# Optimization experiments

Measured on AMD Instinct MI355X. Metric: run time of the kernel, lower is better.

Reference implementation:

```python
import jax, jax.numpy as jnp
import numpy as np

N, E, EP, DIN, H = 100000, 600000, 100000, 128, 128


def _lin_params(key, din, dout):
    k1, k2 = jax.random.split(key)
    bound = 1.0 / np.sqrt(din)
    W = jax.random.uniform(k1, (din, dout), minval=-bound, maxval=bound, dtype=jnp.float32)
    b = jax.random.uniform(k2, (dout,), minval=-bound, maxval=bound, dtype=jnp.float32)
    return W, b


def setup_inputs() -> dict:
    key = jax.random.key(0)
    ks = jax.random.split(key, 12)
    x = jax.random.normal(ks[0], (N, DIN), dtype=jnp.float32)
    edge_attr = jax.random.normal(ks[1], (E, 1), dtype=jnp.float32)
    edge_index = jax.random.randint(ks[2], (2, E), 0, N, dtype=jnp.int64)
    predict_edge_index = jax.random.randint(ks[3], (2, EP), 0, N, dtype=jnp.int64)
    W1, b1 = _lin_params(ks[4], DIN, H)          # GCNConv layer 0
    W2, b2 = _lin_params(ks[5], H, H)            # GCNConv layer 1
    eW1, eb1 = _lin_params(ks[6], H + H + 1, H)  # edge_mlp layer 0
    eW2, eb2 = _lin_params(ks[7], H + H + H, H)  # edge_mlp layer 1
    pW1, pb1 = _lin_params(ks[8], 2 * H, H)      # edge_mlps2
    pW2, pb2 = _lin_params(ks[9], H, H)
    pW3, pb3 = _lin_params(ks[10], H, H)
    pW4, pb4 = _lin_params(ks[11], H, 1)
    return dict(x=x, edge_attr=edge_attr, edge_index=edge_index,
                predict_edge_index=predict_edge_index,
                W1=W1, b1=b1, W2=W2, b2=b2, eW1=eW1, eb1=eb1, eW2=eW2, eb2=eb2,
                pW1=pW1, pb1=pb1, pW2=pW2, pb2=pb2, pW3=pW3, pb3=pb3, pW4=pW4, pb4=pb4)


def _gcn_conv(x, edge_index, W, b):
    # PyG GCNConv: add self-loops, symmetric normalization, aggregate at target.
    src, dst = edge_index[0], edge_index[1]
    loop = jnp.arange(N)
    src2 = jnp.concatenate([src, loop])
    dst2 = jnp.concatenate([dst, loop])
    deg = jax.ops.segment_sum(jnp.ones_like(dst2, dtype=x.dtype), dst2, num_segments=N)
    dinv = jnp.where(deg > 0, jax.lax.rsqrt(deg), 0.0)
    norm = dinv[src2] * dinv[dst2]                 # [E+N]
    h = x @ W                                      # [N, H]
    msg = norm[:, None] * h[src2]                  # gather + scale
    return jax.ops.segment_sum(msg, dst2, num_segments=N) + b


def reference(x, edge_attr, edge_index, predict_edge_index,
              W1, b1, W2, b2, eW1, eb1, eW2, eb2,
              pW1, pb1, pW2, pb2, pW3, pb3, pW4, pb4):
    # layer 0
    x = jax.nn.relu(_gcn_conv(x, edge_index, W1, b1))
    xi, xj = x[edge_index[0]], x[edge_index[1]]
    edge_attr = jax.nn.relu(jnp.concatenate([xi, xj, edge_attr], axis=-1) @ eW1 + eb1)
    # (Sequential already has ReLU; forward applies relu again -- idempotent)
    # layer 1
    x = jax.nn.relu(_gcn_conv(x, edge_index, W2, b2))
    xi, xj = x[edge_index[0]], x[edge_index[1]]
    edge_attr = jax.nn.relu(jnp.concatenate([xi, xj, edge_attr], axis=-1) @ eW2 + eb2)
    # predict_edge
    xi, xj = x[predict_edge_index[0]], x[predict_edge_index[1]]
    y = jnp.concatenate([xi, xj], axis=-1)
    y = jax.nn.relu(y @ pW1 + pb1)
    y = jax.nn.relu(y @ pW2 + pb2)
    y = jax.nn.relu(y @ pW3 + pb3)
    y = jax.nn.relu(y @ pW4 + pb4)
    return y
```

## Files before the change

### kernel.cpp

```cpp
#include <hip/hip_runtime.h>

typedef __attribute__((ext_vector_type(8))) short bf16x8;
typedef __attribute__((ext_vector_type(4))) float f32x4;
typedef __attribute__((ext_vector_type(16))) float f32x16;
typedef __attribute__((ext_vector_type(2))) float f32x2;

__device__ __forceinline__ unsigned bfr16(float x) {
    unsigned u = __float_as_uint(x);
    return (u + 0x7fffu + ((u >> 16) & 1u)) >> 16;
}

union U8 { bf16x8 v; unsigned u[4]; };

__device__ __forceinline__ void frag_from_f32(const float* fp, bf16x8& hi) {
    float4 f0 = *(const float4*)fp;
    float4 f1 = *(const float4*)(fp + 4);
    float fv[8] = {f0.x, f0.y, f0.z, f0.w, f1.x, f1.y, f1.z, f1.w};
    U8 H;
    #pragma unroll
    for (int p = 0; p < 4; p++)
        H.u[p] = bfr16(fv[2 * p]) | (bfr16(fv[2 * p + 1]) << 16);
    hi = H.v;
}

__device__ __forceinline__ bf16x8 frag_from_f8(const unsigned char* p) {
    uint2 q = *(const uint2*)p;
    f32x2 e0 = __builtin_amdgcn_cvt_pk_f32_fp8(q.x, false);
    f32x2 e1 = __builtin_amdgcn_cvt_pk_f32_fp8(q.x, true);
    f32x2 e2 = __builtin_amdgcn_cvt_pk_f32_fp8(q.y, false);
    f32x2 e3 = __builtin_amdgcn_cvt_pk_f32_fp8(q.y, true);
    U8 H;
    H.u[0] = bfr16(e0.x) | (bfr16(e0.y) << 16);
    H.u[1] = bfr16(e1.x) | (bfr16(e1.y) << 16);
    H.u[2] = bfr16(e2.x) | (bfr16(e2.y) << 16);
    H.u[3] = bfr16(e3.x) | (bfr16(e3.y) << 16);
    return H.v;
}

__device__ __forceinline__ void stage_w512(unsigned short* sm, const unsigned short* Wp, int t) {
    const uint4* src = (const uint4*)Wp;
    uint4* dst = (uint4*)sm;
    #pragma unroll
    for (int p = 0; p < 4; p++) dst[t + p * 512] = src[t + p * 512];
}

__device__ __forceinline__ bf16x8 wfrag_lds(const unsigned short* sm, int f, int lane) {
    return *(const bf16x8*)(sm + f * 512 + lane * 8);
}


__device__ __forceinline__ bf16x8 trans32(const f32x16& A, int sb, float4 bva, float4 bvb) {
    float v0 = fmaxf(A[sb + 0] + bva.x, 0.f);
    float v1 = fmaxf(A[sb + 1] + bva.y, 0.f);
    float v2 = fmaxf(A[sb + 2] + bva.z, 0.f);
    float v3 = fmaxf(A[sb + 3] + bva.w, 0.f);
    float v4 = fmaxf(A[sb + 4] + bvb.x, 0.f);
    float v5 = fmaxf(A[sb + 5] + bvb.y, 0.f);
    float v6 = fmaxf(A[sb + 6] + bvb.z, 0.f);
    float v7 = fmaxf(A[sb + 7] + bvb.w, 0.f);
    U8 H;
    H.u[0] = bfr16(v0) | (bfr16(v1) << 16);
    H.u[1] = bfr16(v2) | (bfr16(v3) << 16);
    H.u[2] = bfr16(v4) | (bfr16(v5) << 16);
    H.u[3] = bfr16(v6) | (bfr16(v7) << 16);
    return H.v;
}


__global__ void zero1_k(int* __restrict__ a, int n) {
    int i = blockIdx.x * blockDim.x + threadIdx.x;
    if (i < n) a[i] = 0;
}

__global__ void hist_k(const int* __restrict__ dst, int* __restrict__ deg,
                       int* __restrict__ rank, int E) {
    int e = blockIdx.x * blockDim.x + threadIdx.x;
    if (e < E) rank[e] = atomicAdd(&deg[dst[e]], 1);
}

__global__ void scan1_k(const int* __restrict__ deg, int* __restrict__ rowptr,
                        int* __restrict__ bsum, float* __restrict__ dinv, int n) {
    __shared__ int s[256];
    int tid = threadIdx.x;
    int i = blockIdx.x * 256 + tid;
    int v = (i < n) ? deg[i] : 0;
    s[tid] = v;
    __syncthreads();
    #pragma unroll
    for (int off = 1; off < 256; off <<= 1) {
        int t = (tid >= off) ? s[tid - off] : 0;
        __syncthreads();
        s[tid] += t;
        __syncthreads();
    }
    if (i < n) {
        rowptr[i] = s[tid] - v;
        dinv[i] = rsqrtf((float)(v + 1));
    }
    if (tid == 255) bsum[blockIdx.x] = s[255];
}

__global__ void scan2_k(int* __restrict__ bsum, int nb) {
    __shared__ int s[512];
    int tid = threadIdx.x;
    int v = (tid < nb) ? bsum[tid] : 0;
    s[tid] = v;
    __syncthreads();
    #pragma unroll
    for (int off = 1; off < 512; off <<= 1) {
        int t = (tid >= off) ? s[tid - off] : 0;
        __syncthreads();
        s[tid] += t;
        __syncthreads();
    }
    if (tid < nb) bsum[tid] = s[tid] - v;
}

__global__ void place_k(const int* __restrict__ src, const int* __restrict__ dst,
                        const int* __restrict__ rowptr, const int* __restrict__ bsum,
                        const int* __restrict__ rank, int* __restrict__ csr, int E) {
    int e = blockIdx.x * blockDim.x + threadIdx.x;
    if (e < E) {
        int d = dst[e];
        int pos = rowptr[d] + bsum[d >> 8] + rank[e];
        csr[pos] = src[e];
    }
}

__global__ void wprep6_k(const float* __restrict__ s0, const float* __restrict__ s1,
                         const float* __restrict__ s2, const float* __restrict__ s3,
                         const float* __restrict__ s4, const float* __restrict__ s5,
                         unsigned short* __restrict__ dstBase) {
    const float* W;
    switch (blockIdx.y) {
        case 0: W = s0; break; case 1: W = s1; break; case 2: W = s2; break;
        case 3: W = s3; break; case 4: W = s4; break; default: W = s5; break;
    }
    unsigned short* out = dstBase + (size_t)blockIdx.y * 16384;
    int idx = blockIdx.x * 256 + threadIdx.x;
    if (idx >= 16384) return;
    int k = idx >> 7, c = idx & 127;
    unsigned hr = bfr16(W[k * 128 + c]);
    int pos;
    if (blockIdx.y < 2) {
        int kt = k >> 5, gk = (k >> 3) & 3, j = k & 7;
        int nt = ((c >> 5) << 1) | ((c >> 2) & 1);
        int rho = (((c >> 3) & 3) << 2) | (c & 3);
        int lane = (gk << 4) | rho;
        pos = (kt * 8 + nt) * 512 + lane * 8 + j;
    } else {
        int kk = k >> 4, gk = (k >> 3) & 1, jj = k & 7;
        int ktc = c >> 4, hc = (c >> 3) & 1, jc = c & 7;
        int n = ktc >> 1;
        int reg = ((ktc & 1) << 3) | jc;
        int m = (reg & 3) + 8 * (reg >> 2) + 4 * hc;
        int lane = (gk << 5) | m;
        pos = (kk * 4 + n) * 512 + lane * 8 + jj;
    }
    out[pos] = (unsigned short)hr;
}

#define ACC16(Q)                                                              \
    {                                                                         \
        f32x2 e;                                                              \
        e = __builtin_amdgcn_cvt_pk_f32_fp8((Q).x, false); a0 += e.x; a1 += e.y; \
        e = __builtin_amdgcn_cvt_pk_f32_fp8((Q).x, true);  a2 += e.x; a3 += e.y; \
        e = __builtin_amdgcn_cvt_pk_f32_fp8((Q).y, false); a4 += e.x; a5 += e.y; \
        e = __builtin_amdgcn_cvt_pk_f32_fp8((Q).y, true);  a6 += e.x; a7 += e.y; \
        e = __builtin_amdgcn_cvt_pk_f32_fp8((Q).z, false); a8 += e.x; a9 += e.y; \
        e = __builtin_amdgcn_cvt_pk_f32_fp8((Q).z, true);  a10 += e.x; a11 += e.y; \
        e = __builtin_amdgcn_cvt_pk_f32_fp8((Q).w, false); a12 += e.x; a13 += e.y; \
        e = __builtin_amdgcn_cvt_pk_f32_fp8((Q).w, true);  a14 += e.x; a15 += e.y; \
    }

template<int OUTFMT>
__global__ __launch_bounds__(256)
void gather8_k(const unsigned char* __restrict__ hp, const float* __restrict__ dinv,
               const int* __restrict__ rowptr, const int* __restrict__ bsum,
               const int* __restrict__ deg, const int* __restrict__ csr,
               const float* __restrict__ bias, void* __restrict__ outPtr, int N)
{
    int tid = threadIdx.x;
    int lane = tid & 63;
    int grp = lane >> 3, cl = lane & 7;
    int i = blockIdx.x * 32 + (tid >> 6) * 8 + grp;
    if (i >= N) return;
    int c16 = cl * 16;
    uint4 p = *(const uint4*)(hp + (size_t)i * 128 + c16);
    float a0 = 0.f, a1 = 0.f, a2 = 0.f, a3 = 0.f, a4 = 0.f, a5 = 0.f, a6 = 0.f, a7 = 0.f;
    float a8 = 0.f, a9 = 0.f, a10 = 0.f, a11 = 0.f, a12 = 0.f, a13 = 0.f, a14 = 0.f, a15 = 0.f;
    ACC16(p);
    int beg = rowptr[i] + bsum[i >> 8];
    int dg = deg[i];
    int j = 0;
    for (; j + 7 < dg; j += 8) {
        uint4 q[8];
        #pragma unroll
        for (int u = 0; u < 8; u++) {
            int su = csr[beg + j + u];
            q[u] = *(const uint4*)(hp + (size_t)su * 128 + c16);
        }
        #pragma unroll
        for (int u = 0; u < 8; u++) ACC16(q[u]);
    }
    for (; j + 3 < dg; j += 4) {
        uint4 q[4];
        #pragma unroll
        for (int u = 0; u < 4; u++) {
            int su = csr[beg + j + u];
            q[u] = *(const uint4*)(hp + (size_t)su * 128 + c16);
        }
        #pragma unroll
        for (int u = 0; u < 4; u++) ACC16(q[u]);
    }
    for (; j < dg; j++) {
        int su = csr[beg + j];
        uint4 q0 = *(const uint4*)(hp + (size_t)su * 128 + c16);
        ACC16(q0);
    }
    float di = dinv[i];
    float4 b0 = *(const float4*)(bias + c16);
    float4 b1 = *(const float4*)(bias + c16 + 4);
    float4 b2 = *(const float4*)(bias + c16 + 8);
    float4 b3 = *(const float4*)(bias + c16 + 12);
    float v0  = fmaxf(b0.x + di * a0,  0.f), v1  = fmaxf(b0.y + di * a1,  0.f);
    float v2  = fmaxf(b0.z + di * a2,  0.f), v3  = fmaxf(b0.w + di * a3,  0.f);
    float v4  = fmaxf(b1.x + di * a4,  0.f), v5  = fmaxf(b1.y + di * a5,  0.f);
    float v6  = fmaxf(b1.z + di * a6,  0.f), v7  = fmaxf(b1.w + di * a7,  0.f);
    float v8  = fmaxf(b2.x + di * a8,  0.f), v9  = fmaxf(b2.y + di * a9,  0.f);
    float v10 = fmaxf(b2.z + di * a10, 0.f), v11 = fmaxf(b2.w + di * a11, 0.f);
    float v12 = fmaxf(b3.x + di * a12, 0.f), v13 = fmaxf(b3.y + di * a13, 0.f);
    float v14 = fmaxf(b3.z + di * a14, 0.f), v15 = fmaxf(b3.w + di * a15, 0.f);
    if (OUTFMT == 0) {
        unsigned short* outp = (unsigned short*)outPtr + (size_t)i * 128 + c16;
        uint4 o0, o1;
        o0.x = bfr16(v0)  | (bfr16(v1)  << 16);
        o0.y = bfr16(v2)  | (bfr16(v3)  << 16);
        o0.z = bfr16(v4)  | (bfr16(v5)  << 16);
        o0.w = bfr16(v6)  | (bfr16(v7)  << 16);
        o1.x = bfr16(v8)  | (bfr16(v9)  << 16);
        o1.y = bfr16(v10) | (bfr16(v11) << 16);
        o1.z = bfr16(v12) | (bfr16(v13) << 16);
        o1.w = bfr16(v14) | (bfr16(v15) << 16);
        *(uint4*)outp = o0;
        *(uint4*)(outp + 8) = o1;
    } else {
        int r0 = 0, r1 = 0, r2 = 0, r3 = 0;
        r0 = __builtin_amdgcn_cvt_pk_fp8_f32(v0,  v1,  r0, false);
        r0 = __builtin_amdgcn_cvt_pk_fp8_f32(v2,  v3,  r0, true);
        r1 = __builtin_amdgcn_cvt_pk_fp8_f32(v4,  v5,  r1, false);
        r1 = __builtin_amdgcn_cvt_pk_fp8_f32(v6,  v7,  r1, true);
        r2 = __builtin_amdgcn_cvt_pk_fp8_f32(v8,  v9,  r2, false);
        r2 = __builtin_amdgcn_cvt_pk_fp8_f32(v10, v11, r2, true);
        r3 = __builtin_amdgcn_cvt_pk_fp8_f32(v12, v13, r3, false);
        r3 = __builtin_amdgcn_cvt_pk_fp8_f32(v14, v15, r3, true);
        uint4 o = make_uint4((unsigned)r0, (unsigned)r1, (unsigned)r2, (unsigned)r3);
        *(uint4*)((unsigned char*)outPtr + (size_t)i * 128 + c16) = o;
    }
}

template<int AMODE>
__global__ __launch_bounds__(512)
void rowgemm_k(const void* __restrict__ Asrc, const unsigned short* __restrict__ Wp,
               const float* __restrict__ rowScale, unsigned char* __restrict__ CoutF8, int M)
{
    __shared__ __align__(16) unsigned short smw[16384];
    const int t = threadIdx.x, lane = t & 63, wave = t >> 6;
    const int base = blockIdx.x * 128 + wave * 16;
    const int s = lane & 15, g = lane >> 4, kg = g * 8;
    const int arow = base + s;
    const int rowc = (arow < M) ? arow : (M - 1);

    stage_w512(smw, Wp, t);

    bf16x8 yh[4];
    #pragma unroll
    for (int kt = 0; kt < 4; kt++) {
        if (AMODE == 1)
            yh[kt] = *(const bf16x8*)((const unsigned short*)Asrc + (size_t)rowc * 128 + kt * 32 + kg);
        else
            frag_from_f32((const float*)Asrc + (size_t)rowc * 128 + kt * 32 + kg, yh[kt]);
    }
    __syncthreads();

    f32x4 acc[8];
    #pragma unroll
    for (int nt = 0; nt < 8; nt++) acc[nt] = (f32x4){0.f, 0.f, 0.f, 0.f};

    #pragma unroll
    for (int kt = 0; kt < 4; kt++) {
        #pragma unroll
        for (int nt = 0; nt < 8; nt++) {
            bf16x8 whi = wfrag_lds(smw, kt * 8 + nt, lane);
            acc[nt] = __builtin_amdgcn_mfma_f32_16x16x32_bf16(whi, yh[kt], acc[nt], 0, 0, 0);
        }
    }

    if (arow < M) {
        float sc = rowScale[arow];
        #pragma unroll
        for (int nt = 0; nt < 8; nt++) {
            int cbase = 32 * (nt >> 1) + 8 * g + 4 * (nt & 1);
            int r = 0;
            r = __builtin_amdgcn_cvt_pk_fp8_f32(acc[nt][0] * sc, acc[nt][1] * sc, r, false);
            r = __builtin_amdgcn_cvt_pk_fp8_f32(acc[nt][2] * sc, acc[nt][3] * sc, r, true);
            *(unsigned*)(CoutF8 + (size_t)arow * 128 + cbase) = (unsigned)r;
        }
    }
}

__global__ __launch_bounds__(512)
void mlp_k(const unsigned char* __restrict__ X, const int* __restrict__ psrc, const int* __restrict__ pdst,
           const unsigned short* __restrict__ W1a, const unsigned short* __restrict__ W1b,
           const float* __restrict__ b1, const unsigned short* __restrict__ W2p,
           const float* __restrict__ b2, const unsigned short* __restrict__ W3p,
           const float* __restrict__ b3, const float* __restrict__ w4,
           const float* __restrict__ b4p, float* __restrict__ out, int M)
{
    __shared__ __align__(16) unsigned short smw[2][16384];
    const int t = threadIdx.x, lane = t & 63, wave = t >> 6;
    const int base = blockIdx.x * 256 + wave * 32;
    const int s = lane & 31, h8 = (lane >> 5) * 8;
    const int arow = base + s;
    const int rowc = (arow < M) ? arow : (M - 1);
    const int si = psrc[rowc], sj = pdst[rowc];

    bf16x8 xi[8], xj[8];
    #pragma unroll
    for (int kt = 0; kt < 8; kt++)
        xi[kt] = frag_from_f8(X + (size_t)si * 128 + kt * 16 + h8);
    #pragma unroll
    for (int kt = 0; kt < 8; kt++)
        xj[kt] = frag_from_f8(X + (size_t)sj * 128 + kt * 16 + h8);

    stage_w512(smw[0], W1a, t);
    stage_w512(smw[1], W1b, t);
    __syncthreads();

    f32x16 acc1[4];
    #pragma unroll
    for (int nt = 0; nt < 4; nt++)
        #pragma unroll
        for (int q = 0; q < 16; q++) acc1[nt][q] = 0.f;
    #pragma unroll
    for (int kt = 0; kt < 8; kt++) {
        #pragma unroll
        for (int nt = 0; nt < 4; nt++) {
            bf16x8 wa = wfrag_lds(smw[0], kt * 4 + nt, lane);
            acc1[nt] = __builtin_amdgcn_mfma_f32_32x32x16_bf16(wa, xi[kt], acc1[nt], 0, 0, 0);
            bf16x8 wb = wfrag_lds(smw[1], kt * 4 + nt, lane);
            acc1[nt] = __builtin_amdgcn_mfma_f32_32x32x16_bf16(wb, xj[kt], acc1[nt], 0, 0, 0);
        }
    }
    __syncthreads();

    stage_w512(smw[0], W2p, t);
    stage_w512(smw[1], W3p, t);
    __syncthreads();

    f32x16 acc2[4];
    #pragma unroll
    for (int nt = 0; nt < 4; nt++)
        #pragma unroll
        for (int q = 0; q < 16; q++) acc2[nt][q] = 0.f;
    #pragma unroll
    for (int kt = 0; kt < 8; kt++) {
        float4 bva = *(const float4*)(b1 + kt * 16 + h8);
        float4 bvb = *(const float4*)(b1 + kt * 16 + h8 + 4);
        bf16x8 yh = trans32(acc1[kt >> 1], (kt & 1) * 8, bva, bvb);
        #pragma unroll
        for (int nt = 0; nt < 4; nt++) {
            bf16x8 whi = wfrag_lds(smw[0], kt * 4 + nt, lane);
            acc2[nt] = __builtin_amdgcn_mfma_f32_32x32x16_bf16(whi, yh, acc2[nt], 0, 0, 0);
        }
    }

    f32x16 acc3[4];
    #pragma unroll
    for (int nt = 0; nt < 4; nt++)
        #pragma unroll
        for (int q = 0; q < 16; q++) acc3[nt][q] = 0.f;
    #pragma unroll
    for (int kt = 0; kt < 8; kt++) {
        float4 bva = *(const float4*)(b2 + kt * 16 + h8);
        float4 bvb = *(const float4*)(b2 + kt * 16 + h8 + 4);
        bf16x8 yh = trans32(acc2[kt >> 1], (kt & 1) * 8, bva, bvb);
        #pragma unroll
        for (int nt = 0; nt < 4; nt++) {
            bf16x8 whi = wfrag_lds(smw[1], kt * 4 + nt, lane);
            acc3[nt] = __builtin_amdgcn_mfma_f32_32x32x16_bf16(whi, yh, acc3[nt], 0, 0, 0);
        }
    }

    float p = 0.f;
    #pragma unroll
    for (int nt = 0; nt < 4; nt++) {
        int c1 = 32 * nt + h8;
        int c2 = 32 * nt + 16 + h8;
        float4 b3a = *(const float4*)(b3 + c1);
        float4 b3b = *(const float4*)(b3 + c1 + 4);
        float4 b3c = *(const float4*)(b3 + c2);
        float4 b3d = *(const float4*)(b3 + c2 + 4);
        float4 w4a = *(const float4*)(w4 + c1);
        float4 w4b = *(const float4*)(w4 + c1 + 4);
        float4 w4c = *(const float4*)(w4 + c2);
        float4 w4d = *(const float4*)(w4 + c2 + 4);
        p += fmaxf(acc3[nt][0]  + b3a.x, 0.f) * w4a.x;
        p += fmaxf(acc3[nt][1]  + b3a.y, 0.f) * w4a.y;
        p += fmaxf(acc3[nt][2]  + b3a.z, 0.f) * w4a.z;
        p += fmaxf(acc3[nt][3]  + b3a.w, 0.f) * w4a.w;
        p += fmaxf(acc3[nt][4]  + b3b.x, 0.f) * w4b.x;
        p += fmaxf(acc3[nt][5]  + b3b.y, 0.f) * w4b.y;
        p += fmaxf(acc3[nt][6]  + b3b.z, 0.f) * w4b.z;
        p += fmaxf(acc3[nt][7]  + b3b.w, 0.f) * w4b.w;
        p += fmaxf(acc3[nt][8]  + b3c.x, 0.f) * w4c.x;
        p += fmaxf(acc3[nt][9]  + b3c.y, 0.f) * w4c.y;
        p += fmaxf(acc3[nt][10] + b3c.z, 0.f) * w4c.z;
        p += fmaxf(acc3[nt][11] + b3c.w, 0.f) * w4c.w;
        p += fmaxf(acc3[nt][12] + b3d.x, 0.f) * w4d.x;
        p += fmaxf(acc3[nt][13] + b3d.y, 0.f) * w4d.y;
        p += fmaxf(acc3[nt][14] + b3d.z, 0.f) * w4d.z;
        p += fmaxf(acc3[nt][15] + b3d.w, 0.f) * w4d.w;
    }
    p += __shfl_xor(p, 32, 64);
    if (lane < 32 && arow < M) out[arow] = fmaxf(p + b4p[0], 0.f);
}

extern "C" void kernel_launch(void* const* d_in, const int* in_sizes, int n_in,
                              void* d_out, int out_size, void* d_ws, size_t ws_size,
                              hipStream_t stream)
{
    const float* x   = (const float*)d_in[0];
    const int*   ei  = (const int*)d_in[2];
    const int*   pei = (const int*)d_in[3];
    const float* W1  = (const float*)d_in[4];
    const float* b1  = (const float*)d_in[5];
    const float* W2  = (const float*)d_in[6];
    const float* b2  = (const float*)d_in[7];
    const float* pW1 = (const float*)d_in[12];
    const float* pb1 = (const float*)d_in[13];
    const float* pW2 = (const float*)d_in[14];
    const float* pb2 = (const float*)d_in[15];
    const float* pW3 = (const float*)d_in[16];
    const float* pb3 = (const float*)d_in[17];
    const float* pW4 = (const float*)d_in[18];
    const float* pb4 = (const float*)d_in[19];

    const int N  = in_sizes[0] / 128;
    const int E  = in_sizes[2] / 2;
    const int EP = in_sizes[3] / 2;
    const int Npad = (N + 255) & ~255;

    float*          ws     = (float*)d_ws;
    float*          dinv   = ws;
    unsigned char*  hpF8   = (unsigned char*)(ws + Npad);
    unsigned short* bufB   = (unsigned short*)(hpF8 + (size_t)N * 128);
    unsigned char*  bufC   = (unsigned char*)(bufB + (size_t)N * 128);
    size_t ioff = (((size_t)(bufC + (size_t)N * 128)) + 255) & ~(size_t)255;
    int*   deg    = (int*)ioff;
    int*   rowptr = deg + Npad;
    int*   rank   = rowptr + Npad;
    int*   csr    = rank + E;
    int*   bsum   = csr + E;
    size_t wpOff = ((size_t)(bsum + 512) + 15) & ~(size_t)15;
    unsigned short* wp = (unsigned short*)wpOff;
    unsigned short* W1p  = wp;
    unsigned short* W2p  = wp + 16384;
    unsigned short* P1Ap = wp + 2 * 16384;
    unsigned short* P1Bp = wp + 3 * 16384;
    unsigned short* P2p  = wp + 4 * 16384;
    unsigned short* P3p  = wp + 5 * 16384;
    float* out = (float*)d_out;

    const int* esrc = ei;
    const int* edst = ei + E;
    const int* psrc = pei;
    const int* pdst = pei + EP;

    const int nb = (N + 255) / 256;
    const int gN = (N + 255) / 256;
    const int gE = (E + 255) / 256;
    const int gT = (N + 127) / 128;
    const int gP = (EP + 255) / 256;
    const int gG = (N + 31) / 32;

    zero1_k<<<gN, 256, 0, stream>>>(deg, N);
    hist_k<<<gE, 256, 0, stream>>>(edst, deg, rank, E);
    scan1_k<<<nb, 256, 0, stream>>>(deg, rowptr, bsum, dinv, N);
    scan2_k<<<1, 512, 0, stream>>>(bsum, nb);
    place_k<<<gE, 256, 0, stream>>>(esrc, edst, rowptr, bsum, rank, csr, E);

    wprep6_k<<<dim3(64, 6), 256, 0, stream>>>(W1, W2, pW1, pW1 + 128 * 128, pW2, pW3, wp);

    rowgemm_k<0><<<gT, 512, 0, stream>>>(x, W1p, dinv, hpF8, N);
    gather8_k<0><<<gG, 256, 0, stream>>>(hpF8, dinv, rowptr, bsum, deg, csr, b1, bufB, N);

    rowgemm_k<1><<<gT, 512, 0, stream>>>(bufB, W2p, dinv, hpF8, N);
    gather8_k<1><<<gG, 256, 0, stream>>>(hpF8, dinv, rowptr, bsum, deg, csr, b2, bufC, N);

    mlp_k<<<gP, 512, 0, stream>>>(bufC, psrc, pdst, P1Ap, P1Bp, pb1, P2p, pb2, P3p, pb3,
                                  pW4, pb4, out, EP);
}
```

Measured before the change: 156.1 us.

## Sort nodes by in-degree to balance gather workload across lanes

Adds a counting-sort pass (per-block degree histogram, scan of the bins, placement) that builds a node permutation grouped by in-degree. Both gather kernels then process nodes in that order, so the 8-lane groups within a wavefront see similar degrees and diverge less. The cost is four extra small kernel launches and an extra indirection per node, and output rows are written in scattered order, which loses some write locality.

```diff
diff --git a/kernel.cpp b/kernel.cpp
--- a/kernel.cpp
+++ b/kernel.cpp
@@ -124,6 +124,52 @@
         int d = dst[e];
         int pos = rowptr[d] + bsum[d >> 8] + rank[e];
         csr[pos] = src[e];
+    }
+}
+
+
+__global__ void dhist_k(const int* __restrict__ deg, int* __restrict__ brank,
+                        int* __restrict__ gbin, int n) {
+    __shared__ int bins[128];
+    int tid = threadIdx.x;
+    if (tid < 128) bins[tid] = 0;
+    __syncthreads();
+    int i = blockIdx.x * 256 + tid;
+    if (i < n) {
+        int b = min(deg[i], 127);
+        brank[i] = atomicAdd(&bins[b], 1);
+    }
+    __syncthreads();
+    if (tid < 128) gbin[tid * gridDim.x + blockIdx.x] = bins[tid];
+}
+
+__global__ void pscan_k(int* __restrict__ g, int* __restrict__ gsum, int total) {
+    __shared__ int s[256];
+    int tid = threadIdx.x;
+    int idx = blockIdx.x * 256 + tid;
+    int v = (idx < total) ? g[idx] : 0;
+    s[tid] = v;
+    __syncthreads();
+    #pragma unroll
+    for (int off = 1; off < 256; off <<= 1) {
+        int t = (tid >= off) ? s[tid - off] : 0;
+        __syncthreads();
+        s[tid] += t;
+        __syncthreads();
+    }
+    if (idx < total) g[idx] = s[tid] - v;
+    if (tid == 255) gsum[blockIdx.x] = s[255];
+}
+
+__global__ void dplace_k(const int* __restrict__ deg, const int* __restrict__ brank,
+                         const int* __restrict__ gbin, const int* __restrict__ gsum,
+                         int* __restrict__ order, int n, int nb) {
+    int i = blockIdx.x * 256 + threadIdx.x;
+    if (i < n) {
+        int b = min(deg[i], 127);
+        int flat = b * nb + (i >> 8);
+        int pos = gbin[flat] + gsum[flat >> 8] + brank[i];
+        order[pos] = i;
     }
 }
 
@@ -178,13 +224,15 @@
 void gather8_k(const unsigned char* __restrict__ hp, const float* __restrict__ dinv,
                const int* __restrict__ rowptr, const int* __restrict__ bsum,
                const int* __restrict__ deg, const int* __restrict__ csr,
-               const float* __restrict__ bias, void* __restrict__ outPtr, int N)
+               const int* __restrict__ order, const float* __restrict__ bias,
+               void* __restrict__ outPtr, int N)
 {
     int tid = threadIdx.x;
     int lane = tid & 63;
     int grp = lane >> 3, cl = lane & 7;
-    int i = blockIdx.x * 32 + (tid >> 6) * 8 + grp;
-    if (i >= N) return;
+    int idx = blockIdx.x * 32 + (tid >> 6) * 8 + grp;
+    if (idx >= N) return;
+    int i = order[idx];
     int c16 = cl * 16;
     uint4 p = *(const uint4*)(hp + (size_t)i * 128 + c16);
     float a0 = 0.f, a1 = 0.f, a2 = 0.f, a3 = 0.f, a4 = 0.f, a5 = 0.f, a6 = 0.f, a7 = 0.f;
@@ -461,8 +509,13 @@
     int*   rowptr = deg + Npad;
     int*   rank   = rowptr + Npad;
     int*   csr    = rank + E;
-    int*   bsum   = csr + E;
-    size_t wpOff = ((size_t)(bsum + 512) + 15) & ~(size_t)15;
+    int*   brank  = csr + E;
+    int*   order  = brank + Npad;
+    int*   bsum   = order + Npad;
+    int*   gsum   = bsum + 512;
+    int*   gbin   = gsum + 512;
+    const int nb = (N + 255) / 256;
+    size_t wpOff = ((size_t)(gbin + 128 * nb + 256) + 15) & ~(size_t)15;
     unsigned short* wp = (unsigned short*)wpOff;
     unsigned short* W1p  = wp;
     unsigned short* W2p  = wp + 16384;
@@ -477,26 +530,32 @@
     const int* psrc = pei;
     const int* pdst = pei + EP;
 
-    const int nb = (N + 255) / 256;
     const int gN = (N + 255) / 256;
     const int gE = (E + 255) / 256;
     const int gT = (N + 127) / 128;
     const int gP = (EP + 255) / 256;
     const int gG = (N + 31) / 32;
+    const int totalBins = 128 * nb;
+    const int gBins = (totalBins + 255) / 256;
 
     zero1_k<<<gN, 256, 0, stream>>>(deg, N);
     hist_k<<<gE, 256, 0, stream>>>(edst, deg, rank, E);
-    scan1_k<<<nb, 256, 0, stream>>>(deg, rowptr, bsum, dinv, N);
-    scan2_k<<<1, 512, 0, stream>>>(bsum, nb);
+    scan1_k<<<gN, 256, 0, stream>>>(deg, rowptr, bsum, dinv, N);
+    scan2_k<<<1, 512, 0, stream>>>(bsum, gN);
     place_k<<<gE, 256, 0, stream>>>(esrc, edst, rowptr, bsum, rank, csr, E);
 
+    dhist_k<<<gN, 256, 0, stream>>>(deg, brank, gbin, N);
+    pscan_k<<<gBins, 256, 0, stream>>>(gbin, gsum, totalBins);
+    scan2_k<<<1, 512, 0, stream>>>(gsum, gBins);
+    dplace_k<<<gN, 256, 0, stream>>>(deg, brank, gbin, gsum, order, N, nb);
+
     wprep6_k<<<dim3(64, 6), 256, 0, stream>>>(W1, W2, pW1, pW1 + 128 * 128, pW2, pW3, wp);
 
     rowgemm_k<0><<<gT, 512, 0, stream>>>(x, W1p, dinv, hpF8, N);
-    gather8_k<0><<<gG, 256, 0, stream>>>(hpF8, dinv, rowptr, bsum, deg, csr, b1, bufB, N);
+    gather8_k<0><<<gG, 256, 0, stream>>>(hpF8, dinv, rowptr, bsum, deg, csr, order, b1, bufB, N);
 
     rowgemm_k<1><<<gT, 512, 0, stream>>>(bufB, W2p, dinv, hpF8, N);
-    gather8_k<1><<<gG, 256, 0, stream>>>(hpF8, dinv, rowptr, bsum, deg, csr, b2, bufC, N);
+    gather8_k<1><<<gG, 256, 0, stream>>>(hpF8, dinv, rowptr, bsum, deg, csr, order, b2, bufC, N);
 
     mlp_k<<<gP, 512, 0, stream>>>(bufC, psrc, pdst, P1Ap, P1Bp, pb1, P2p, pb2, P3p, pb3,
                                   pW4, pb4, out, EP);
```

Result: slower. 160.4 us (+2.7%).
